# Kernel optimization log

Measured on AMD Instinct MI355X. Metric: run time of the kernel, lower is better.

Reference implementation:

```python
import jax, jax.numpy as jnp
import numpy as np

NEG_SLOPE_MLP = 0.1   # F.leaky_relu(x, 0.1) used throughout the repo
NEG_SLOPE_GAT = 0.2   # PyG GATv2Conv default negative_slope
HEADS = 2
OUT = 8


def lrelu(x):
    return jax.nn.leaky_relu(x, NEG_SLOPE_MLP)


def gatv2_conv(x, src, dst, e_attr, wl, bl, wr, br, we, att, bias):
    """PyG-style GATv2Conv with edge features, concat heads.
    x: [N, Din], src/dst: [E], e_attr: [E, 2]
    wl/wr: [heads*out, Din], we: [heads*out, 2], att: [heads, out], bias: [heads*out]
    """
    N = x.shape[0]
    xl = (x @ wl.T + bl).reshape(N, HEADS, OUT)   # source transform
    xr = (x @ wr.T + br).reshape(N, HEADS, OUT)   # target transform
    e = (e_attr @ we.T).reshape(-1, HEADS, OUT)
    m = jax.nn.leaky_relu(xl[src] + xr[dst] + e, NEG_SLOPE_GAT)   # [E, H, O]
    logits = jnp.einsum('ehd,hd->eh', m, att)                      # [E, H]
    # numerically-stable segment softmax over incoming edges of each dst node
    mx = jax.ops.segment_max(logits, dst, num_segments=N)          # [N, H]
    a = jnp.exp(logits - mx[dst])
    denom = jax.ops.segment_sum(a, dst, num_segments=N)
    alpha = a / (denom[dst] + 1e-16)                               # [E, H]
    out = jax.ops.segment_sum(xl[src] * alpha[..., None], dst, num_segments=N)
    return out.reshape(N, HEADS * OUT) + bias                      # [N, 16]


def setup_inputs() -> dict:
    key = jax.random.key(0)
    ks = iter(jax.random.split(key, 64))
    N, E = 250000, 5000000
    inp = {
        'x': jax.random.normal(next(ks), (N, 3), jnp.float32),
        'edge_index': jax.random.randint(next(ks), (2, E), 0, N, jnp.int32),
        'edge_attr': jax.random.normal(next(ks), (E, 2), jnp.float32),
        'meta_data': jax.random.normal(next(ks), (6,), jnp.float32),
    }
    shapes = dict(
        ft1_w=(8, 3), ft1_b=(8,), ft2_w=(8, 8), ft2_b=(8,),
        g1_wl=(16, 8), g1_bl=(16,), g1_wr=(16, 8), g1_br=(16,), g1_we=(16, 2), g1_att=(2, 8), g1_bias=(16,),
        g2_wl=(16, 16), g2_bl=(16,), g2_wr=(16, 16), g2_br=(16,), g2_we=(16, 2), g2_att=(2, 8), g2_bias=(16,),
        sp1_w=(64, 16), sp1_b=(64,), sp2_w=(16, 64), sp2_b=(16,),
        me_w=(8, 6), me_b=(8,),
        fc1_w=(24, 24), fc1_b=(24,), fc2_w=(8, 24), fc2_b=(8,), fc3_w=(3, 8), fc3_b=(3,),
    )
    for name, shp in shapes.items():
        inp[name] = 0.2 * jax.random.normal(next(ks), shp, jnp.float32)
    return inp


def reference(x, edge_index, edge_attr, meta_data,
              ft1_w, ft1_b, ft2_w, ft2_b,
              g1_wl, g1_bl, g1_wr, g1_br, g1_we, g1_att, g1_bias,
              g2_wl, g2_bl, g2_wr, g2_br, g2_we, g2_att, g2_bias,
              sp1_w, sp1_b, sp2_w, sp2_b, me_w, me_b,
              fc1_w, fc1_b, fc2_w, fc2_b, fc3_w, fc3_b):
    src, dst = edge_index[0], edge_index[1]
    # tiny per-node MLP feature transform
    h = lrelu(x @ ft1_w.T + ft1_b)
    h = lrelu(h @ ft2_w.T + ft2_b)                              # [N, 8]
    # 2-layer GATv2 block (activation between layers)
    h = gatv2_conv(h, src, dst, edge_attr, g1_wl, g1_bl, g1_wr, g1_br, g1_we, g1_att, g1_bias)
    h = lrelu(h)
    h = gatv2_conv(h, src, dst, edge_attr, g2_wl, g2_bl, g2_wr, g2_br, g2_we, g2_att, g2_bias)  # [N, 16]
    # sum pool over all nodes + small MLP
    p = h.sum(axis=0)                                           # [16]
    p = lrelu(p @ sp1_w.T + sp1_b)
    p = p @ sp2_w.T + sp2_b                                     # [16]
    # meta data encoder
    m = lrelu(meta_data @ me_w.T + me_b)                        # [8]
    z = jnp.concatenate([p, m], axis=0)                         # [24]
    z = lrelu(z @ fc1_w.T + fc1_b)
    z = lrelu(z @ fc2_w.T + fc2_b)
    # dropout is identity in eval/reference mode
    z = z @ fc3_w.T + fc3_b                                     # [3]
    return jax.nn.softmax(z[None, :], axis=1)                   # [1, 3]
```

## Files before the change

kernel.cpp:

```cpp
#include <hip/hip_runtime.h>
#include <hip/hip_bf16.h>
#include <hip/hip_fp16.h>
#include <math.h>


#define HO 16
#define BSHIFT 8
#define BNODES 256
#define PT 512
#define PCHUNK 6144
#define CAP2 6016

typedef __attribute__((ext_vector_type(2))) float v2f;

__device__ __forceinline__ float lrelu(float x, float s) { return x > 0.f ? x : s * x; }

__device__ __forceinline__ uint2 pack_fp8x8(const float* v) {
    int a = __builtin_amdgcn_cvt_pk_fp8_f32(v[0], v[1], 0, false);
    a     = __builtin_amdgcn_cvt_pk_fp8_f32(v[2], v[3], a, true);
    int b = __builtin_amdgcn_cvt_pk_fp8_f32(v[4], v[5], 0, false);
    b     = __builtin_amdgcn_cvt_pk_fp8_f32(v[6], v[7], b, true);
    return make_uint2((unsigned int)a, (unsigned int)b);
}

__device__ __forceinline__ void unpack_fp8x8(uint2 u, float* v) {
    v2f f0 = __builtin_amdgcn_cvt_pk_f32_fp8((int)u.x, false);
    v2f f1 = __builtin_amdgcn_cvt_pk_f32_fp8((int)u.x, true);
    v2f f2 = __builtin_amdgcn_cvt_pk_f32_fp8((int)u.y, false);
    v2f f3 = __builtin_amdgcn_cvt_pk_f32_fp8((int)u.y, true);
    v[0]=f0.x; v[1]=f0.y; v[2]=f1.x; v[3]=f1.y;
    v[4]=f2.x; v[5]=f2.y; v[6]=f3.x; v[7]=f3.y;
}

__global__ void __launch_bounds__(256) node_l1(
    const float* __restrict__ x,
    const float* __restrict__ ft1_w, const float* __restrict__ ft1_b,
    const float* __restrict__ ft2_w, const float* __restrict__ ft2_b,
    const float* __restrict__ wl, const float* __restrict__ bl,
    const float* __restrict__ wr, const float* __restrict__ br,
    uint2* __restrict__ xlA, float* __restrict__ xr, int N)
{
    int n = blockIdx.x * 256 + threadIdx.x;
    if (n >= N) return;
    float x0 = x[3*n], x1 = x[3*n+1], x2 = x[3*n+2];
    float h1[8];
#pragma unroll
    for (int j = 0; j < 8; j++) {
        float a = ft1_w[3*j]*x0 + ft1_w[3*j+1]*x1 + ft1_w[3*j+2]*x2 + ft1_b[j];
        h1[j] = lrelu(a, 0.1f);
    }
    float h2[8];
#pragma unroll
    for (int j = 0; j < 8; j++) {
        float a = ft2_b[j];
#pragma unroll
        for (int k = 0; k < 8; k++) a += ft2_w[8*j+k]*h1[k];
        h2[j] = lrelu(a, 0.1f);
    }
    float ol[HO], orr[HO];
#pragma unroll
    for (int j = 0; j < HO; j++) {
        float a = bl[j], b = br[j];
#pragma unroll
        for (int k = 0; k < 8; k++) { a += wl[8*j+k]*h2[k]; b += wr[8*j+k]*h2[k]; }
        ol[j] = a; orr[j] = b;
    }
    uint2 p0 = pack_fp8x8(ol);
    uint2 p1 = pack_fp8x8(ol + 8);
    ((uint4*)xlA)[n] = make_uint4(p0.x, p0.y, p1.x, p1.y);
    float4* xr4 = (float4*)(xr + (size_t)n*HO);
#pragma unroll
    for (int q = 0; q < 4; q++)
        xr4[q] = make_float4(orr[4*q], orr[4*q+1], orr[4*q+2], orr[4*q+3]);
}

__global__ void __launch_bounds__(256) k_binit(int* __restrict__ bcur)
{
    int b = blockIdx.x * 256 + threadIdx.x;
    if (b < 1024) bcur[b] = b * CAP2;
}

__global__ void __launch_bounds__(PT) k_part(
    const int* __restrict__ src, const int* __restrict__ dst,
    const float* __restrict__ eattr, int* __restrict__ bcur,
    uint2* __restrict__ grecs, int E)
{
    __shared__ int hist[1024], lofs[1024], gofs[1024], lcur[1024];
    __shared__ int scan_s[PT];
    __shared__ uint2 srecs[PCHUNK];
    __shared__ unsigned short bid[PCHUNK];
    int t = threadIdx.x;
    int base = blockIdx.x * PCHUNK;
    int cnt = E - base; if (cnt > PCHUNK) cnt = PCHUNK;

    for (int b = t; b < 1024; b += PT) hist[b] = 0;
    __syncthreads();
    for (int i = t; i < cnt; i += PT)
        atomicAdd(&hist[dst[base + i] >> BSHIFT], 1);
    __syncthreads();
    int h0 = hist[2*t], h1 = hist[2*t+1];
    int pair = h0 + h1;
    scan_s[t] = pair;
    __syncthreads();
    for (int off = 1; off < PT; off <<= 1) {
        int add = (t >= off) ? scan_s[t - off] : 0;
        __syncthreads();
        scan_s[t] += add;
        __syncthreads();
    }
    int pbase = scan_s[t] - pair;
    lofs[2*t]   = pbase;
    lofs[2*t+1] = pbase + h0;
    __syncthreads();
    for (int b = t; b < 1024; b += PT) {
        int c = hist[b];
        int g = (c > 0) ? atomicAdd(&bcur[b], c) : 0;
        gofs[b] = g - lofs[b];
        lcur[b] = 0;
    }
    __syncthreads();
    for (int i = t; i < cnt; i += PT) {
        int e = base + i;
        int d = dst[e];
        int b = d >> BSHIFT;
        float2 ea = ((const float2*)eattr)[e];
        __half2 hv = __floats2half2_rn(ea.x, ea.y);
        unsigned int eb = *reinterpret_cast<unsigned int*>(&hv);
        int q = atomicAdd(&lcur[b], 1);
        int idx = lofs[b] + q;
        srecs[idx] = make_uint2(((unsigned int)src[e] << 8) | (unsigned int)(d & (BNODES-1)), eb);
        bid[idx] = (unsigned short)b;
    }
    __syncthreads();
    for (int i = t; i < cnt; i += PT) {
        int b = bid[i];
        int pos = gofs[b] + i;
        if (pos < (b + 1) * CAP2) grecs[pos] = srecs[i];
    }
}

__global__ void __launch_bounds__(256) k_fine(
    const int* __restrict__ bcur, uint2* recs,
    int* __restrict__ rowS, int* __restrict__ rowE, int N)
{
    __shared__ uint2 rout[CAP2];
    __shared__ int lhist[256], lsc[256], lcur2[256];
    int b = blockIdx.x;
    int bstart = b * CAP2;
    int cnt = bcur[b] - bstart;
    if (cnt > CAP2) cnt = CAP2;
    if (cnt < 0) cnt = 0;
    int t = threadIdx.x;
    lhist[t] = 0;
    __syncthreads();
    for (int i = t; i < cnt; i += 256)
        atomicAdd(&lhist[recs[bstart + i].x & (BNODES-1)], 1);
    __syncthreads();
    int v = lhist[t];
    lsc[t] = v;
    __syncthreads();
    for (int off = 1; off < 256; off <<= 1) {
        int add = (t >= off) ? lsc[t - off] : 0;
        __syncthreads();
        lsc[t] += add;
        __syncthreads();
    }
    int ex = lsc[t] - v;
    lcur2[t] = ex;
    int n = (b << BSHIFT) + t;
    if (n < N) { rowS[n] = bstart + ex; rowE[n] = bstart + ex + v; }
    __syncthreads();
    for (int i = t; i < cnt; i += 256) {
        uint2 r = recs[bstart + i];
        int p = atomicAdd(&lcur2[r.x & (BNODES-1)], 1);
        rout[p] = make_uint2(r.x >> 8, r.y);
    }
    __syncthreads();
    for (int i = t; i < cnt; i += 256)
        recs[bstart + i] = rout[i];
}

struct AggState { float m, s, acc[8]; };

__device__ __forceinline__ void agg_edge(
    AggState& st, const float* va, const float* xd,
    const float* w0, const float* w1, const float* at,
    float ea0, float ea1)
{
    float lg = 0.f;
#pragma unroll
    for (int o = 0; o < 8; o++) {
        float mv = va[o] + xd[o] + (w0[o]*ea0 + w1[o]*ea1);
        mv = mv > 0.f ? mv : 0.2f*mv;
        lg += mv * at[o];
    }
    float nm = fmaxf(st.m, lg);
    float sc = __expf(st.m - nm);
    float wv = __expf(lg - nm);
    st.s = st.s*sc + wv;
#pragma unroll
    for (int o = 0; o < 8; o++) st.acc[o] = st.acc[o]*sc + wv*va[o];
    st.m = nm;
}

__device__ __forceinline__ void agg_node_head(
    int n, int h,
    const int* __restrict__ rowS, const int* __restrict__ rowE,
    const uint2* __restrict__ recs,
    const uint2* __restrict__ xl8, const float* __restrict__ xr,
    const float* __restrict__ we, const float* __restrict__ att,
    const float* __restrict__ bias, float* out)
{
    int kb = h*8;
    float xd[8], w0[8], w1[8], at[8];
    {
        const float4* xrp = (const float4*)(xr + (size_t)n*HO + kb);
        float4 d0 = xrp[0], d1 = xrp[1];
        xd[0]=d0.x; xd[1]=d0.y; xd[2]=d0.z; xd[3]=d0.w;
        xd[4]=d1.x; xd[5]=d1.y; xd[6]=d1.z; xd[7]=d1.w;
    }
#pragma unroll
    for (int o = 0; o < 8; o++) {
        w0[o] = we[2*(kb+o)];
        w1[o] = we[2*(kb+o)+1];
        at[o] = att[kb+o];
    }
    AggState st;
    st.m = -INFINITY; st.s = 0.f;
#pragma unroll
    for (int o = 0; o < 8; o++) st.acc[o] = 0.f;

    int i = rowS[n], end = rowE[n];
    for (; i + 4 <= end; i += 4) {
        uint2 rA = recs[i], rB = recs[i+1], rC = recs[i+2], rD = recs[i+3];
        uint2 gA = xl8[(size_t)rA.x*2 + h];
        uint2 gB = xl8[(size_t)rB.x*2 + h];
        uint2 gC = xl8[(size_t)rC.x*2 + h];
        uint2 gD = xl8[(size_t)rD.x*2 + h];
        float vA[8], vB[8], vC[8], vD[8];
        unpack_fp8x8(gA, vA); unpack_fp8x8(gB, vB);
        unpack_fp8x8(gC, vC); unpack_fp8x8(gD, vD);
        __half2 hA = *reinterpret_cast<__half2*>(&rA.y);
        __half2 hB = *reinterpret_cast<__half2*>(&rB.y);
        __half2 hC = *reinterpret_cast<__half2*>(&rC.y);
        __half2 hD = *reinterpret_cast<__half2*>(&rD.y);
        agg_edge(st, vA, xd, w0, w1, at, __low2float(hA), __high2float(hA));
        agg_edge(st, vB, xd, w0, w1, at, __low2float(hB), __high2float(hB));
        agg_edge(st, vC, xd, w0, w1, at, __low2float(hC), __high2float(hC));
        agg_edge(st, vD, xd, w0, w1, at, __low2float(hD), __high2float(hD));
    }
    for (; i < end; i++) {
        uint2 rA = recs[i];
        uint2 gA = xl8[(size_t)rA.x*2 + h];
        float vA[8];
        unpack_fp8x8(gA, vA);
        __half2 hA = *reinterpret_cast<__half2*>(&rA.y);
        agg_edge(st, vA, xd, w0, w1, at, __low2float(hA), __high2float(hA));
    }
    float inv = 1.f/(st.s + 1e-16f);
#pragma unroll
    for (int o = 0; o < 8; o++) out[o] = st.acc[o]*inv + bias[kb+o];
}

__global__ void __launch_bounds__(256) node_agg_l1(
    const int* __restrict__ rowS, const int* __restrict__ rowE,
    const uint2* __restrict__ recs,
    const uint2* __restrict__ xlA, float* xr,
    const float* __restrict__ we, const float* __restrict__ att,
    const float* __restrict__ bias,
    const float* __restrict__ wl2, const float* __restrict__ bl2,
    const float* __restrict__ wr2, const float* __restrict__ br2,
    uint2* __restrict__ xlB, int N)
{
    int tid = blockIdx.x * 256 + threadIdx.x;
    int n = tid >> 1, h = tid & 1;
    if (n >= N) return;
    int kb = h*8;
    float out[8];
    agg_node_head(n, h, rowS, rowE, recs, xlA, xr, we, att, bias, out);
    float hh[8];
#pragma unroll
    for (int o = 0; o < 8; o++) hh[o] = lrelu(out[o], 0.1f);
    float hfull[HO];
#pragma unroll
    for (int o = 0; o < 8; o++) {
        float hp = __shfl_xor(hh[o], 1, 64);
        hfull[kb + o] = hh[o];
        hfull[(kb ^ 8) + o] = hp;
    }
    float ol[8], orr[8];
#pragma unroll
    for (int jo = 0; jo < 8; jo++) {
        int j = kb + jo;
        float a = bl2[j], b = br2[j];
#pragma unroll
        for (int k = 0; k < HO; k++) { a += wl2[HO*j+k]*hfull[k]; b += wr2[HO*j+k]*hfull[k]; }
        ol[jo] = a; orr[jo] = b;
    }
    xlB[(size_t)n*2 + h] = pack_fp8x8(ol);
    float4* xr4 = (float4*)(xr + (size_t)n*HO + kb);
    xr4[0] = make_float4(orr[0], orr[1], orr[2], orr[3]);
    xr4[1] = make_float4(orr[4], orr[5], orr[6], orr[7]);
}

__global__ void __launch_bounds__(256) node_agg_l2(
    const int* __restrict__ rowS, const int* __restrict__ rowE,
    const uint2* __restrict__ recs,
    const uint2* __restrict__ xlB, const float* __restrict__ xr,
    const float* __restrict__ we, const float* __restrict__ att,
    const float* __restrict__ bias, float* __restrict__ partials, int pstride, int N)
{
    int tid = blockIdx.x * 256 + threadIdx.x;
    int n = tid >> 1, h = tid & 1;
    float out[8];
    if (n < N) {
        agg_node_head(n, h, rowS, rowE, recs, xlB, xr, we, att, bias, out);
    } else {
#pragma unroll
        for (int o = 0; o < 8; o++) out[o] = 0.f;
    }
#pragma unroll
    for (int off = 32; off >= 2; off >>= 1) {
#pragma unroll
        for (int o = 0; o < 8; o++) out[o] += __shfl_down(out[o], off, 64);
    }
    __shared__ float sm[4][2][8];
    int wave = threadIdx.x >> 6, lane = threadIdx.x & 63;
    if (lane < 2) {
#pragma unroll
        for (int o = 0; o < 8; o++) sm[wave][lane][o] = out[o];
    }
    __syncthreads();
    if (threadIdx.x < 16) {
        int hh = threadIdx.x >> 3, oo = threadIdx.x & 7;
        float t = sm[0][hh][oo] + sm[1][hh][oo] + sm[2][hh][oo] + sm[3][hh][oo];
        partials[(size_t)(hh*8 + oo) * pstride + blockIdx.x] = t;
    }
}

__global__ void __launch_bounds__(256) k_reduce(
    const float* __restrict__ partials, int pstride, int nparts,
    float* __restrict__ pool)
{
    __shared__ float s[256];
    int c = blockIdx.x;
    int t = threadIdx.x;
    const float* col = partials + (size_t)c * pstride;
    float acc = 0.f;
    for (int r = t; r < nparts; r += 256) acc += col[r];
    s[t] = acc;
    __syncthreads();
#pragma unroll
    for (int off = 128; off > 0; off >>= 1) {
        if (t < off) s[t] += s[t + off];
        __syncthreads();
    }
    if (t == 0) pool[c] = s[0];
}

__global__ void __launch_bounds__(64) final_mlp(
    const float* __restrict__ pool, const float* __restrict__ meta,
    const float* __restrict__ sp1_w, const float* __restrict__ sp1_b,
    const float* __restrict__ sp2_w, const float* __restrict__ sp2_b,
    const float* __restrict__ me_w, const float* __restrict__ me_b,
    const float* __restrict__ fc1_w, const float* __restrict__ fc1_b,
    const float* __restrict__ fc2_w, const float* __restrict__ fc2_b,
    const float* __restrict__ fc3_w, const float* __restrict__ fc3_b,
    float* __restrict__ out)
{
    __shared__ float s1[64], zb[24], z1[24], z2[8];
    int t = threadIdx.x;
    {
        float acc = sp1_b[t];
        for (int k = 0; k < 16; k++) acc += pool[k]*sp1_w[t*16+k];
        s1[t] = lrelu(acc, 0.1f);
    }
    __syncthreads();
    if (t < 16) {
        float acc = sp2_b[t];
        for (int k = 0; k < 64; k++) acc += s1[k]*sp2_w[t*64+k];
        zb[t] = acc;
    } else if (t < 24) {
        int j = t - 16;
        float acc = me_b[j];
        for (int k = 0; k < 6; k++) acc += meta[k]*me_w[j*6+k];
        zb[t] = lrelu(acc, 0.1f);
    }
    __syncthreads();
    if (t < 24) {
        float acc = fc1_b[t];
        for (int k = 0; k < 24; k++) acc += zb[k]*fc1_w[t*24+k];
        z1[t] = lrelu(acc, 0.1f);
    }
    __syncthreads();
    if (t < 8) {
        float acc = fc2_b[t];
        for (int k = 0; k < 24; k++) acc += z1[k]*fc2_w[t*24+k];
        z2[t] = lrelu(acc, 0.1f);
    }
    __syncthreads();
    if (t == 0) {
        float z3[3]; float mxv = -1e30f;
        for (int j = 0; j < 3; j++) {
            float acc = fc3_b[j];
            for (int k = 0; k < 8; k++) acc += z2[k]*fc3_w[j*8+k];
            z3[j] = acc; mxv = fmaxf(mxv, acc);
        }
        float s = 0.f;
        for (int j = 0; j < 3; j++) { z3[j] = __expf(z3[j]-mxv); s += z3[j]; }
        for (int j = 0; j < 3; j++) out[j] = z3[j]/s;
    }
}

extern "C" void kernel_launch(void* const* d_in, const int* in_sizes, int n_in,
                              void* d_out, int out_size, void* d_ws, size_t ws_size,
                              hipStream_t stream)
{
    const float* x      = (const float*)d_in[0];
    const int*   eidx   = (const int*)  d_in[1];
    const float* eattr  = (const float*)d_in[2];
    const float* meta   = (const float*)d_in[3];
    const float* ft1_w  = (const float*)d_in[4];
    const float* ft1_b  = (const float*)d_in[5];
    const float* ft2_w  = (const float*)d_in[6];
    const float* ft2_b  = (const float*)d_in[7];
    const float* g1_wl  = (const float*)d_in[8];
    const float* g1_bl  = (const float*)d_in[9];
    const float* g1_wr  = (const float*)d_in[10];
    const float* g1_br  = (const float*)d_in[11];
    const float* g1_we  = (const float*)d_in[12];
    const float* g1_att = (const float*)d_in[13];
    const float* g1_bias= (const float*)d_in[14];
    const float* g2_wl  = (const float*)d_in[15];
    const float* g2_bl  = (const float*)d_in[16];
    const float* g2_wr  = (const float*)d_in[17];
    const float* g2_br  = (const float*)d_in[18];
    const float* g2_we  = (const float*)d_in[19];
    const float* g2_att = (const float*)d_in[20];
    const float* g2_bias= (const float*)d_in[21];
    const float* sp1_w  = (const float*)d_in[22];
    const float* sp1_b  = (const float*)d_in[23];
    const float* sp2_w  = (const float*)d_in[24];
    const float* sp2_b  = (const float*)d_in[25];
    const float* me_w   = (const float*)d_in[26];
    const float* me_b   = (const float*)d_in[27];
    const float* fc1_w  = (const float*)d_in[28];
    const float* fc1_b  = (const float*)d_in[29];
    const float* fc2_w  = (const float*)d_in[30];
    const float* fc2_b  = (const float*)d_in[31];
    const float* fc3_w  = (const float*)d_in[32];
    const float* fc3_b  = (const float*)d_in[33];
    float* out = (float*)d_out;

    const int N = in_sizes[0] / 3;
    const int E = in_sizes[2] / 2;
    const int* src = eidx;
    const int* dst = eidx + E;

    const int BN    = (N + 255) / 256;
    const int BN2   = (2*N + 255) / 256;
    const int NBUCK = (N + BNODES - 1) >> BSHIFT;
    const int BP    = (E + PCHUNK - 1) / PCHUNK;
    const int pstride = (BN2 + 63) & ~63;

    char* w = (char*)d_ws;
    size_t off = 0;
    auto take = [&](size_t bytes) { size_t o = off; off += (bytes + 255) & ~(size_t)255; return o; };
    int*    rowS     = (int*)   (w + take((size_t)4*N));
    int*    rowE     = (int*)   (w + take((size_t)4*N));
    int*    bcur     = (int*)   (w + take(4096));
    float*  pool     = (float*) (w + take(64));
    float*  partials = (float*) (w + take((size_t)4*16*pstride));
    uint2*  recs     = (uint2*) (w + take((size_t)8*NBUCK*CAP2));
    uint2*  xlA      = (uint2*) (w + take((size_t)16*N));
    uint2*  xlB      = (uint2*) (w + take((size_t)16*N));
    float*  xr       = (float*) (w + take((size_t)64*N));

    node_l1<<<BN, 256, 0, stream>>>(x, ft1_w, ft1_b, ft2_w, ft2_b,
                                    g1_wl, g1_bl, g1_wr, g1_br, xlA, xr, N);
    k_binit<<<4, 256, 0, stream>>>(bcur);
    k_part<<<BP, PT, 0, stream>>>(src, dst, eattr, bcur, recs, E);
    k_fine<<<NBUCK, 256, 0, stream>>>(bcur, recs, rowS, rowE, N);

    node_agg_l1<<<BN2, 256, 0, stream>>>(rowS, rowE, recs, xlA, xr,
                                         g1_we, g1_att, g1_bias,
                                         g2_wl, g2_bl, g2_wr, g2_br, xlB, N);
    node_agg_l2<<<BN2, 256, 0, stream>>>(rowS, rowE, recs, xlB, xr,
                                         g2_we, g2_att, g2_bias, partials, pstride, N);
    k_reduce<<<16, 256, 0, stream>>>(partials, pstride, BN2, pool);
    final_mlp<<<1, 64, 0, stream>>>(pool, meta, sp1_w, sp1_b, sp2_w, sp2_b,
                                    me_w, me_b, fc1_w, fc1_b, fc2_w, fc2_b,
                                    fc3_w, fc3_b, out);
}
```

Baseline: 420.9 us.

## Split each node-head edge loop across two threads with online-softmax merge

Each node-head is now handled by two threads that process alternate incoming edges, keeping partial online-softmax state and merging via lane shuffles. The 4-edge batch now applies a single rescale per group instead of per edge. In layer 1 the two threads divide the following left/right linear transforms between them. This doubles thread count and shortens per-thread serial edge chains (avg ~20 edges) to raise memory-level parallelism, at the cost of extra shuffles, more partial-sum blocks and duplicated loads of xr and weights.

```diff
diff --git a/kernel.cpp b/kernel.cpp
--- a/kernel.cpp
+++ b/kernel.cpp
@@ -182,7 +182,7 @@
 
 struct AggState { float m, s, acc[8]; };
 
-__device__ __forceinline__ void agg_edge(
+__device__ __forceinline__ void agg_edge1(
     AggState& st, const float* va, const float* xd,
     const float* w0, const float* w1, const float* at,
     float ea0, float ea1)
@@ -203,63 +203,99 @@
     st.m = nm;
 }
 
-__device__ __forceinline__ void agg_node_head(
-    int n, int h,
+__device__ __forceinline__ void agg_partial(
+    int n, int h, int half,
     const int* __restrict__ rowS, const int* __restrict__ rowE,
     const uint2* __restrict__ recs,
     const uint2* __restrict__ xl8, const float* __restrict__ xr,
     const float* __restrict__ we, const float* __restrict__ att,
-    const float* __restrict__ bias, float* out)
+    AggState& st, float* xd)
 {
     int kb = h*8;
-    float xd[8], w0[8], w1[8], at[8];
     {
         const float4* xrp = (const float4*)(xr + (size_t)n*HO + kb);
         float4 d0 = xrp[0], d1 = xrp[1];
         xd[0]=d0.x; xd[1]=d0.y; xd[2]=d0.z; xd[3]=d0.w;
         xd[4]=d1.x; xd[5]=d1.y; xd[6]=d1.z; xd[7]=d1.w;
     }
+    float w0[8], w1[8], at[8];
 #pragma unroll
     for (int o = 0; o < 8; o++) {
         w0[o] = we[2*(kb+o)];
         w1[o] = we[2*(kb+o)+1];
         at[o] = att[kb+o];
     }
-    AggState st;
     st.m = -INFINITY; st.s = 0.f;
 #pragma unroll
     for (int o = 0; o < 8; o++) st.acc[o] = 0.f;
 
-    int i = rowS[n], end = rowE[n];
-    for (; i + 4 <= end; i += 4) {
-        uint2 rA = recs[i], rB = recs[i+1], rC = recs[i+2], rD = recs[i+3];
-        uint2 gA = xl8[(size_t)rA.x*2 + h];
-        uint2 gB = xl8[(size_t)rB.x*2 + h];
-        uint2 gC = xl8[(size_t)rC.x*2 + h];
-        uint2 gD = xl8[(size_t)rD.x*2 + h];
-        float vA[8], vB[8], vC[8], vD[8];
-        unpack_fp8x8(gA, vA); unpack_fp8x8(gB, vB);
-        unpack_fp8x8(gC, vC); unpack_fp8x8(gD, vD);
-        __half2 hA = *reinterpret_cast<__half2*>(&rA.y);
-        __half2 hB = *reinterpret_cast<__half2*>(&rB.y);
-        __half2 hC = *reinterpret_cast<__half2*>(&rC.y);
-        __half2 hD = *reinterpret_cast<__half2*>(&rD.y);
-        agg_edge(st, vA, xd, w0, w1, at, __low2float(hA), __high2float(hA));
-        agg_edge(st, vB, xd, w0, w1, at, __low2float(hB), __high2float(hB));
-        agg_edge(st, vC, xd, w0, w1, at, __low2float(hC), __high2float(hC));
-        agg_edge(st, vD, xd, w0, w1, at, __low2float(hD), __high2float(hD));
-    }
-    for (; i < end; i++) {
-        uint2 rA = recs[i];
-        uint2 gA = xl8[(size_t)rA.x*2 + h];
-        float vA[8];
-        unpack_fp8x8(gA, vA);
-        __half2 hA = *reinterpret_cast<__half2*>(&rA.y);
-        agg_edge(st, vA, xd, w0, w1, at, __low2float(hA), __high2float(hA));
-    }
-    float inv = 1.f/(st.s + 1e-16f);
-#pragma unroll
-    for (int o = 0; o < 8; o++) out[o] = st.acc[o]*inv + bias[kb+o];
+    int i = rowS[n] + half, end = rowE[n];
+    for (; i + 6 < end; i += 8) {
+        uint2 r0 = recs[i], r1 = recs[i+2], r2 = recs[i+4], r3 = recs[i+6];
+        uint2 g0 = xl8[(size_t)r0.x*2 + h];
+        uint2 g1 = xl8[(size_t)r1.x*2 + h];
+        uint2 g2 = xl8[(size_t)r2.x*2 + h];
+        uint2 g3 = xl8[(size_t)r3.x*2 + h];
+        float v0[8], v1[8], v2[8], v3[8];
+        unpack_fp8x8(g0, v0); unpack_fp8x8(g1, v1);
+        unpack_fp8x8(g2, v2); unpack_fp8x8(g3, v3);
+        __half2 e0 = *reinterpret_cast<__half2*>(&r0.y);
+        __half2 e1 = *reinterpret_cast<__half2*>(&r1.y);
+        __half2 e2 = *reinterpret_cast<__half2*>(&r2.y);
+        __half2 e3 = *reinterpret_cast<__half2*>(&r3.y);
+        float lg0 = 0.f, lg1 = 0.f, lg2 = 0.f, lg3 = 0.f;
+        float a0 = __low2float(e0), b0 = __high2float(e0);
+        float a1 = __low2float(e1), b1 = __high2float(e1);
+        float a2 = __low2float(e2), b2 = __high2float(e2);
+        float a3 = __low2float(e3), b3 = __high2float(e3);
+#pragma unroll
+        for (int o = 0; o < 8; o++) {
+            float m0 = v0[o] + xd[o] + (w0[o]*a0 + w1[o]*b0);
+            float m1 = v1[o] + xd[o] + (w0[o]*a1 + w1[o]*b1);
+            float m2 = v2[o] + xd[o] + (w0[o]*a2 + w1[o]*b2);
+            float m3 = v3[o] + xd[o] + (w0[o]*a3 + w1[o]*b3);
+            m0 = m0 > 0.f ? m0 : 0.2f*m0;
+            m1 = m1 > 0.f ? m1 : 0.2f*m1;
+            m2 = m2 > 0.f ? m2 : 0.2f*m2;
+            m3 = m3 > 0.f ? m3 : 0.2f*m3;
+            lg0 += m0*at[o]; lg1 += m1*at[o]; lg2 += m2*at[o]; lg3 += m3*at[o];
+        }
+        float m4 = fmaxf(fmaxf(lg0, lg1), fmaxf(lg2, lg3));
+        float nm = fmaxf(st.m, m4);
+        float sc = __expf(st.m - nm);
+        float q0 = __expf(lg0 - nm), q1 = __expf(lg1 - nm);
+        float q2 = __expf(lg2 - nm), q3 = __expf(lg3 - nm);
+        st.s = st.s*sc + (q0 + q1 + q2 + q3);
+#pragma unroll
+        for (int o = 0; o < 8; o++)
+            st.acc[o] = st.acc[o]*sc + q0*v0[o] + q1*v1[o] + q2*v2[o] + q3*v3[o];
+        st.m = nm;
+    }
+    for (; i < end; i += 2) {
+        uint2 r = recs[i];
+        uint2 g = xl8[(size_t)r.x*2 + h];
+        float v[8];
+        unpack_fp8x8(g, v);
+        __half2 ev = *reinterpret_cast<__half2*>(&r.y);
+        agg_edge1(st, v, xd, w0, w1, at, __low2float(ev), __high2float(ev));
+    }
+}
+
+__device__ __forceinline__ void merge_finalize(
+    AggState& st, const float* __restrict__ bias, int kb, float* out)
+{
+    float mp = __shfl_xor(st.m, 1, 64);
+    float sp = __shfl_xor(st.s, 1, 64);
+    float nm = fmaxf(st.m, mp);
+    float sc1 = 0.f, sc2 = 0.f;
+    if (nm > -INFINITY) { sc1 = __expf(st.m - nm); sc2 = __expf(mp - nm); }
+    float sM = st.s*sc1 + sp*sc2;
+    float inv = 1.f/(sM + 1e-16f);
+#pragma unroll
+    for (int o = 0; o < 8; o++) {
+        float ap = __shfl_xor(st.acc[o], 1, 64);
+        out[o] = (st.acc[o]*sc1 + ap*sc2)*inv + bias[kb+o];
+    }
 }
 
 __global__ void __launch_bounds__(256) node_agg_l1(
@@ -273,34 +309,41 @@
     uint2* __restrict__ xlB, int N)
 {
     int tid = blockIdx.x * 256 + threadIdx.x;
-    int n = tid >> 1, h = tid & 1;
+    int n = tid >> 2, h = (tid >> 1) & 1, half = tid & 1;
     if (n >= N) return;
     int kb = h*8;
+    AggState st; float xd[8];
+    agg_partial(n, h, half, rowS, rowE, recs, xlA, xr, we, att, st, xd);
     float out[8];
-    agg_node_head(n, h, rowS, rowE, recs, xlA, xr, we, att, bias, out);
+    merge_finalize(st, bias, kb, out);
     float hh[8];
 #pragma unroll
     for (int o = 0; o < 8; o++) hh[o] = lrelu(out[o], 0.1f);
     float hfull[HO];
 #pragma unroll
     for (int o = 0; o < 8; o++) {
-        float hp = __shfl_xor(hh[o], 1, 64);
+        float hp = __shfl_xor(hh[o], 2, 64);
         hfull[kb + o] = hh[o];
         hfull[(kb ^ 8) + o] = hp;
     }
-    float ol[8], orr[8];
+    const float* wm = half ? wr2 : wl2;
+    const float* bm = half ? br2 : bl2;
+    float o8[8];
 #pragma unroll
     for (int jo = 0; jo < 8; jo++) {
         int j = kb + jo;
-        float a = bl2[j], b = br2[j];
-#pragma unroll
-        for (int k = 0; k < HO; k++) { a += wl2[HO*j+k]*hfull[k]; b += wr2[HO*j+k]*hfull[k]; }
-        ol[jo] = a; orr[jo] = b;
-    }
-    xlB[(size_t)n*2 + h] = pack_fp8x8(ol);
-    float4* xr4 = (float4*)(xr + (size_t)n*HO + kb);
-    xr4[0] = make_float4(orr[0], orr[1], orr[2], orr[3]);
-    xr4[1] = make_float4(orr[4], orr[5], orr[6], orr[7]);
+        float a = bm[j];
+#pragma unroll
+        for (int k = 0; k < HO; k++) a += wm[HO*j+k]*hfull[k];
+        o8[jo] = a;
+    }
+    if (half == 0) {
+        xlB[(size_t)n*2 + h] = pack_fp8x8(o8);
+    } else {
+        float4* xr4 = (float4*)(xr + (size_t)n*HO + kb);
+        xr4[0] = make_float4(o8[0], o8[1], o8[2], o8[3]);
+        xr4[1] = make_float4(o8[4], o8[5], o8[6], o8[7]);
+    }
 }
 
 __global__ void __launch_bounds__(256) node_agg_l2(
@@ -311,24 +354,30 @@
     const float* __restrict__ bias, float* __restrict__ partials, int pstride, int N)
 {
     int tid = blockIdx.x * 256 + threadIdx.x;
-    int n = tid >> 1, h = tid & 1;
+    int n = tid >> 2, h = (tid >> 1) & 1, half = tid & 1;
     float out[8];
     if (n < N) {
-        agg_node_head(n, h, rowS, rowE, recs, xlB, xr, we, att, bias, out);
+        AggState st; float xd[8];
+        agg_partial(n, h, half, rowS, rowE, recs, xlB, xr, we, att, st, xd);
+        merge_finalize(st, bias, h*8, out);
+        if (half) {
+#pragma unroll
+            for (int o = 0; o < 8; o++) out[o] = 0.f;
+        }
     } else {
 #pragma unroll
         for (int o = 0; o < 8; o++) out[o] = 0.f;
     }
 #pragma unroll
-    for (int off = 32; off >= 2; off >>= 1) {
+    for (int off = 32; off >= 4; off >>= 1) {
 #pragma unroll
         for (int o = 0; o < 8; o++) out[o] += __shfl_down(out[o], off, 64);
     }
     __shared__ float sm[4][2][8];
     int wave = threadIdx.x >> 6, lane = threadIdx.x & 63;
-    if (lane < 2) {
-#pragma unroll
-        for (int o = 0; o < 8; o++) sm[wave][lane][o] = out[o];
+    if (lane == 0 || lane == 2) {
+#pragma unroll
+        for (int o = 0; o < 8; o++) sm[wave][lane >> 1][o] = out[o];
     }
     __syncthreads();
     if (threadIdx.x < 16) {
@@ -458,10 +507,10 @@
     const int* dst = eidx + E;
 
     const int BN    = (N + 255) / 256;
-    const int BN2   = (2*N + 255) / 256;
+    const int BN4   = (4*N + 255) / 256;
     const int NBUCK = (N + BNODES - 1) >> BSHIFT;
     const int BP    = (E + PCHUNK - 1) / PCHUNK;
-    const int pstride = (BN2 + 63) & ~63;
+    const int pstride = (BN4 + 63) & ~63;
 
     char* w = (char*)d_ws;
     size_t off = 0;
@@ -482,12 +531,12 @@
     k_part<<<BP, PT, 0, stream>>>(src, dst, eattr, bcur, recs, E);
     k_fine<<<NBUCK, 256, 0, stream>>>(bcur, recs, rowS, rowE, N);
 
-    node_agg_l1<<<BN2, 256, 0, stream>>>(rowS, rowE, recs, xlA, xr,
+    node_agg_l1<<<BN4, 256, 0, stream>>>(rowS, rowE, recs, xlA, xr,
                                          g1_we, g1_att, g1_bias,
                                          g2_wl, g2_bl, g2_wr, g2_br, xlB, N);
-    node_agg_l2<<<BN2, 256, 0, stream>>>(rowS, rowE, recs, xlB, xr,
+    node_agg_l2<<<BN4, 256, 0, stream>>>(rowS, rowE, recs, xlB, xr,
                                          g2_we, g2_att, g2_bias, partials, pstride, N);
-    k_reduce<<<16, 256, 0, stream>>>(partials, pstride, BN2, pool);
+    k_reduce<<<16, 256, 0, stream>>>(partials, pstride, BN4, pool);
     final_mlp<<<1, 64, 0, stream>>>(pool, meta, sp1_w, sp1_b, sp2_w, sp2_b,
                                     me_w, me_b, fc1_w, fc1_b, fc2_w, fc2_b,
                                     fc3_w, fc3_b, out);
```

Result: slower. 442.7 us (+5.2%).
